# Kernel tuning notes

Measured on AMD Instinct MI355X. Metric: run time of the kernel, lower is better.

The kernel has to match this reference:

```python
import jax, jax.numpy as jnp
import numpy as np

EPS = 1e-12
SIMILARITY = 'dot'  # non-tensor forward arg, closed over


def setup_inputs() -> dict:
    key = jax.random.key(0)
    k1, k2, k3, k4 = jax.random.split(key, 4)
    N, M, D = 4096, 8192, 512
    x = jax.random.normal(k1, (N, D), dtype=jnp.float32)
    x_n = jax.random.normal(k2, (M, D), dtype=jnp.float32)
    # Linear(D, 3) params
    W = jax.random.normal(k3, (3, D), dtype=jnp.float32) * (1.0 / np.sqrt(D))
    bias = jax.random.normal(k4, (3,), dtype=jnp.float32) * 0.01
    return {"x": x, "x_n": x_n, "W": W, "bias": bias}


def _sim_matrix(x, x_n, similarity):
    if similarity == 'l2':
        d2 = (jnp.sum(x * x, 1)[:, None] - 2.0 * (x @ x_n.T)
              + jnp.sum(x_n * x_n, 1)[None, :])
        return -jnp.sqrt(jnp.maximum(d2, 0.0))
    elif similarity == 'l1':
        return -jnp.sum(jnp.abs(x[:, None, :] - x_n[None, :, :]), axis=-1)
    elif similarity == 'dot':
        return (x @ x_n.T) / x.shape[1]
    elif similarity == 'cos':
        xn = x / jnp.linalg.norm(x, axis=1, keepdims=True)
        yn = x_n / jnp.linalg.norm(x_n, axis=1, keepdims=True)
        return xn @ yn.T


def reference(x, x_n, W, bias):
    # pointwise params from a Linear(D,3)+Sigmoid head, clamped to (eps, 1-eps)
    p = jnp.clip(jax.nn.sigmoid(x @ W.T + bias), EPS, 1.0 - EPS)  # [N,3]
    a = p[:, 0:1]
    b = p[:, 1:2]
    s = p[:, 2:3]
    b = a + b * (1.0 - a)

    sim = _sim_matrix(x, x_n, SIMILARITY)                # [N,M]
    smin = jnp.min(sim, axis=1, keepdims=True)
    smax = jnp.max(sim, axis=1, keepdims=True)
    sim_norm = (sim - smin) / (smax - smin)

    # x != x_n -> plain row max (torch.equal branch is False)
    top_sims = jnp.max(sim_norm, axis=1, keepdims=True)  # [N,1]
    a = jnp.minimum(a, top_sims) - EPS

    num = jnp.maximum(jnp.abs(sim_norm - a) ** (1.0 / s), EPS)
    denom = num + jnp.maximum(jnp.abs(b - sim_norm) ** (1.0 / s), EPS)
    soft_mask = num / denom

    lo = sim_norm < a
    hi = sim_norm > b
    soft_mask = jnp.where(lo, 0.0, jnp.where(hi, 1.0, soft_mask))
    # safe log: masked-to-0 entries give -inf forward, zero grad (matches torch)
    safe = jnp.where(lo, 1.0, soft_mask)
    log_mask = jnp.where(lo, -jnp.inf, jnp.log(safe))
    return sim + log_mask
```

## Files before the change

### kernel.cpp

```cpp
#include <hip/hip_runtime.h>
#include <hip/hip_fp16.h>
#include <math.h>

#define EPSF 1e-12f
#define NEG_HUGE (-1e30f)

typedef _Float16 half8_t __attribute__((ext_vector_type(8)));
typedef _Float16 half4_t __attribute__((ext_vector_type(4)));
typedef float floatx4 __attribute__((ext_vector_type(4)));

__device__ __forceinline__ float sigmoid_stable(float v) {
    if (v >= 0.0f) {
        return 1.0f / (1.0f + expf(-v));
    } else {
        float e = expf(v);
        return e / (1.0f + e);
    }
}

__global__ __launch_bounds__(64) void row_params_kernel(
    const float* __restrict__ x, const float* __restrict__ W,
    const float* __restrict__ bias,
    float* __restrict__ aeff, float* __restrict__ bnew, float* __restrict__ tinv)
{
    const int r = blockIdx.x;
    const int l = threadIdx.x;
    const float* xr = x + (size_t)r * 512;
    float s0 = 0.0f, s1 = 0.0f, s2 = 0.0f;
#pragma unroll
    for (int i = 0; i < 8; ++i) {
        int e = l * 8 + i;
        float xv = xr[e];
        s0 = fmaf(xv, W[e], s0);
        s1 = fmaf(xv, W[512 + e], s1);
        s2 = fmaf(xv, W[1024 + e], s2);
    }
#pragma unroll
    for (int off = 32; off > 0; off >>= 1) {
        s0 += __shfl_xor(s0, off);
        s1 += __shfl_xor(s1, off);
        s2 += __shfl_xor(s2, off);
    }
    if (l == 0) {
        float p0 = fminf(fmaxf(sigmoid_stable(s0 + bias[0]), EPSF), 1.0f);
        float p1 = fminf(fmaxf(sigmoid_stable(s1 + bias[1]), EPSF), 1.0f);
        float p2 = fminf(fmaxf(sigmoid_stable(s2 + bias[2]), EPSF), 1.0f);
        float b = p0 + p1 * (1.0f - p0);
        float ae = fminf(p0, 1.0f) - EPSF;
        aeff[r] = ae;
        bnew[r] = b;
        tinv[r] = 1.0f / p2;
    }
}

__global__ __launch_bounds__(256) void split_both_kernel(
    const float* __restrict__ x, const float* __restrict__ xn,
    _Float16* __restrict__ A2, _Float16* __restrict__ B2)
{
    int idx = blockIdx.x * 256 + threadIdx.x;
    int row = idx >> 7;
    int c = (idx & 127) << 2;
    const float* src;
    _Float16* dst;
    bool isB;
    if (row < 4096) {
        src = x + (size_t)row * 512 + c;
        dst = A2 + (size_t)row * 1536 + c;
        isB = false;
    } else {
        int r = row - 4096;
        src = xn + (size_t)r * 512 + c;
        dst = B2 + (size_t)r * 1536 + c;
        isB = true;
    }
    float4 v = *(const float4*)src;
    _Float16 h0 = (_Float16)v.x, h1 = (_Float16)v.y,
             h2 = (_Float16)v.z, h3 = (_Float16)v.w;
    half4_t hv = {h0, h1, h2, h3};
    half4_t lv = {(_Float16)(v.x - (float)h0), (_Float16)(v.y - (float)h1),
                  (_Float16)(v.z - (float)h2), (_Float16)(v.w - (float)h3)};
    *(half4_t*)(dst) = hv;
    *(half4_t*)(dst + 512)  = isB ? lv : hv;
    *(half4_t*)(dst + 1024) = isB ? hv : lv;
}

__device__ __forceinline__ void load_tile_row16(
    const _Float16* gbase, _Float16* lds_base, int lane)
{
    const _Float16* g = gbase + (size_t)(lane >> 2) * 1536 + (size_t)(lane & 3) * 8;
    __builtin_amdgcn_global_load_lds(
        (const __attribute__((address_space(1))) unsigned int*)g,
        (__attribute__((address_space(3))) unsigned int*)lds_base,
        16, 0, 0);
}

__global__ __launch_bounds__(256) void mfma_gemm_kernel(
    const _Float16* __restrict__ A, const _Float16* __restrict__ B,
    float* __restrict__ C,
    float* __restrict__ pmin, float* __restrict__ pmax)
{
    constexpr int Kp = 1536;
    constexpr int N = 8192;
    __shared__ __align__(16) _Float16 As[128 * 32];
    __shared__ __align__(16) _Float16 Bs[128 * 32];

    const int t = threadIdx.x;
    const int wave = t >> 6;
    const int lane = t & 63;
    const int bx = blockIdx.x;
    const int by = blockIdx.y;

    const _Float16* Abase = A + (size_t)(by * 128 + wave * 16) * Kp;
    const _Float16* Bbase = B + (size_t)(bx * 128 + wave * 16) * Kp;
    _Float16* AsW0 = &As[(wave * 16) * 32];
    _Float16* AsW1 = &As[(64 + wave * 16) * 32];
    _Float16* BsW0 = &Bs[(wave * 16) * 32];
    _Float16* BsW1 = &Bs[(64 + wave * 16) * 32];
    const size_t rs64 = (size_t)64 * Kp;

    const int wm = (wave >> 1) * 64;
    const int wn = (wave & 1) * 64;
    const _Float16* aptr = &As[(wm + (lane & 15)) * 32 + (lane >> 4) * 8];
    const _Float16* bptr = &Bs[(wn + (lane & 15)) * 32 + (lane >> 4) * 8];

    floatx4 acc[4][4] = {};

    for (int kt = 0; kt < Kp / 32; ++kt) {
        const _Float16* Ak = Abase + kt * 32;
        const _Float16* Bk = Bbase + kt * 32;
        load_tile_row16(Ak, AsW0, lane);
        load_tile_row16(Ak + rs64, AsW1, lane);
        load_tile_row16(Bk, BsW0, lane);
        load_tile_row16(Bk + rs64, BsW1, lane);
        __syncthreads();

        half8_t af[4], bf[4];
#pragma unroll
        for (int i = 0; i < 4; ++i) af[i] = *(const half8_t*)(aptr + i * 16 * 32);
#pragma unroll
        for (int j = 0; j < 4; ++j) bf[j] = *(const half8_t*)(bptr + j * 16 * 32);
#pragma unroll
        for (int i = 0; i < 4; ++i)
#pragma unroll
            for (int j = 0; j < 4; ++j)
                acc[i][j] = __builtin_amdgcn_mfma_f32_16x16x32_f16(
                    af[i], bf[j], acc[i][j], 0, 0, 0);
        __syncthreads();
    }

    const float sc = 1.0f / 512.0f;
    const int row0 = by * 128 + wm + (lane >> 4) * 4;
    const int col0 = bx * 128 + wn + (lane & 15);
#pragma unroll
    for (int i = 0; i < 4; ++i) {
#pragma unroll
        for (int r = 0; r < 4; ++r) {
            float* cp = C + (size_t)(row0 + i * 16 + r) * N + col0;
#pragma unroll
            for (int j = 0; j < 4; ++j)
                cp[j * 16] = acc[i][j][r] * sc;
        }
    }

    float mnv[4][4], mxv[4][4];
#pragma unroll
    for (int i = 0; i < 4; ++i)
#pragma unroll
        for (int r = 0; r < 4; ++r) {
            float lo = fminf(fminf(acc[i][0][r], acc[i][1][r]),
                             fminf(acc[i][2][r], acc[i][3][r]));
            float hi = fmaxf(fmaxf(acc[i][0][r], acc[i][1][r]),
                             fmaxf(acc[i][2][r], acc[i][3][r]));
            mnv[i][r] = lo * sc;
            mxv[i][r] = hi * sc;
        }
#pragma unroll
    for (int off = 1; off < 16; off <<= 1)
#pragma unroll
        for (int i = 0; i < 4; ++i)
#pragma unroll
            for (int r = 0; r < 4; ++r) {
                mnv[i][r] = fminf(mnv[i][r], __shfl_xor(mnv[i][r], off));
                mxv[i][r] = fmaxf(mxv[i][r], __shfl_xor(mxv[i][r], off));
            }
    if ((lane & 15) == 0) {
        const int pb = bx * 2 + (wave & 1);
#pragma unroll
        for (int i = 0; i < 4; ++i)
#pragma unroll
            for (int r = 0; r < 4; ++r) {
                size_t row = (size_t)(row0 + i * 16 + r);
                pmin[(row << 7) + pb] = mnv[i][r];
                pmax[(row << 7) + pb] = mxv[i][r];
            }
    }
}

__global__ __launch_bounds__(64) void minmax_reduce_kernel(
    const float* __restrict__ pmin, const float* __restrict__ pmax,
    float* __restrict__ smin, float* __restrict__ smax)
{
    const int r = blockIdx.x;
    const int l = threadIdx.x;
    const float* bmin = pmin + ((size_t)r << 7);
    const float* bmax = pmax + ((size_t)r << 7);
    float mn = fminf(bmin[l], bmin[l + 64]);
    float mx = fmaxf(bmax[l], bmax[l + 64]);
#pragma unroll
    for (int off = 32; off > 0; off >>= 1) {
        mn = fminf(mn, __shfl_xor(mn, off));
        mx = fmaxf(mx, __shfl_xor(mx, off));
    }
    if (l == 0) {
        smin[r] = mn;
        smax[r] = mx;
    }
}

#define BM 128
#define BN 128
#define BK 16
__global__ __launch_bounds__(256) void sgemm_nt_kernel(
    const float* __restrict__ A, const float* __restrict__ B,
    float* __restrict__ C)
{
    const int K = 512;
    const int N = 8192;
    __shared__ float As[BK][BM];
    __shared__ float Bs[BK][BN];
    const int t = threadIdx.x;
    const int bx = blockIdx.x, by = blockIdx.y;
    const int m0 = t >> 2;
    const int kq = (t & 3) << 2;
    const float* Ap = A + ((size_t)(by * BM + m0) * K + kq);
    const float* Bp = B + ((size_t)(bx * BN + m0) * K + kq);
    const int tx = t & 15, ty = t >> 4;
    float acc[8][8] = {};
    float4 a0 = *(const float4*)(Ap), a1 = *(const float4*)(Ap + (size_t)64 * K);
    float4 b0 = *(const float4*)(Bp), b1 = *(const float4*)(Bp + (size_t)64 * K);
    for (int kt = 0; kt < K / BK; ++kt) {
        As[kq + 0][m0] = a0.x; As[kq + 1][m0] = a0.y; As[kq + 2][m0] = a0.z; As[kq + 3][m0] = a0.w;
        As[kq + 0][m0 + 64] = a1.x; As[kq + 1][m0 + 64] = a1.y; As[kq + 2][m0 + 64] = a1.z; As[kq + 3][m0 + 64] = a1.w;
        Bs[kq + 0][m0] = b0.x; Bs[kq + 1][m0] = b0.y; Bs[kq + 2][m0] = b0.z; Bs[kq + 3][m0] = b0.w;
        Bs[kq + 0][m0 + 64] = b1.x; Bs[kq + 1][m0 + 64] = b1.y; Bs[kq + 2][m0 + 64] = b1.z; Bs[kq + 3][m0 + 64] = b1.w;
        __syncthreads();
        if (kt + 1 < K / BK) {
            const float* Ap2 = Ap + (size_t)(kt + 1) * BK;
            const float* Bp2 = Bp + (size_t)(kt + 1) * BK;
            a0 = *(const float4*)(Ap2); a1 = *(const float4*)(Ap2 + (size_t)64 * K);
            b0 = *(const float4*)(Bp2); b1 = *(const float4*)(Bp2 + (size_t)64 * K);
        }
#pragma unroll
        for (int k = 0; k < BK; ++k) {
            float4 xa0 = *(const float4*)(&As[k][ty * 8]);
            float4 xa1 = *(const float4*)(&As[k][ty * 8 + 4]);
            float4 yb0 = *(const float4*)(&Bs[k][tx * 8]);
            float4 yb1 = *(const float4*)(&Bs[k][tx * 8 + 4]);
            float av[8] = {xa0.x, xa0.y, xa0.z, xa0.w, xa1.x, xa1.y, xa1.z, xa1.w};
            float bv[8] = {yb0.x, yb0.y, yb0.z, yb0.w, yb1.x, yb1.y, yb1.z, yb1.w};
#pragma unroll
            for (int i = 0; i < 8; ++i)
#pragma unroll
                for (int j = 0; j < 8; ++j)
                    acc[i][j] = fmaf(av[i], bv[j], acc[i][j]);
        }
        __syncthreads();
    }
    const float sc = 1.0f / 512.0f;
    const int gm = by * BM + ty * 8, gn = bx * BN + tx * 8;
#pragma unroll
    for (int i = 0; i < 8; ++i) {
        float4 o0 = make_float4(acc[i][0] * sc, acc[i][1] * sc, acc[i][2] * sc, acc[i][3] * sc);
        float4 o1 = make_float4(acc[i][4] * sc, acc[i][5] * sc, acc[i][6] * sc, acc[i][7] * sc);
        float* cp = C + (size_t)(gm + i) * N + gn;
        *(float4*)(cp) = o0;
        *(float4*)(cp + 4) = o1;
    }
}

__global__ __launch_bounds__(256) void row_minmax_kernel(
    const float* __restrict__ C, float* __restrict__ smin, float* __restrict__ smax)
{
    const int r = blockIdx.x;
    const float4* row = (const float4*)(C + (size_t)r * 8192);
    float mn = INFINITY, mx = -INFINITY;
#pragma unroll
    for (int i = 0; i < 8; ++i) {
        float4 v = row[threadIdx.x + i * 256];
        mn = fminf(mn, fminf(fminf(v.x, v.y), fminf(v.z, v.w)));
        mx = fmaxf(mx, fmaxf(fmaxf(v.x, v.y), fmaxf(v.z, v.w)));
    }
#pragma unroll
    for (int off = 32; off > 0; off >>= 1) {
        mn = fminf(mn, __shfl_xor(mn, off));
        mx = fmaxf(mx, __shfl_xor(mx, off));
    }
    __shared__ float smn[4], smx[4];
    if ((threadIdx.x & 63) == 0) {
        smn[threadIdx.x >> 6] = mn;
        smx[threadIdx.x >> 6] = mx;
    }
    __syncthreads();
    if (threadIdx.x == 0) {
        mn = fminf(fminf(smn[0], smn[1]), fminf(smn[2], smn[3]));
        mx = fmaxf(fmaxf(smx[0], smx[1]), fmaxf(smx[2], smx[3]));
        smin[r] = mn;
        smax[r] = mx;
    }
}

__device__ __forceinline__ float fast_pow(float x, float t) {
    return __expf(t * __logf(x));
}

__global__ __launch_bounds__(256) void epilogue_kernel(
    float* __restrict__ C,
    const float* __restrict__ aeff, const float* __restrict__ bnew,
    const float* __restrict__ tinv,
    const float* __restrict__ smin, const float* __restrict__ smax)
{
    const int r = blockIdx.y;
    const int c4 = blockIdx.x * 256 + threadIdx.x;
    const float a = aeff[r];
    const float b = bnew[r];
    const float t = tinv[r];
    const float mn = smin[r];
    const float range = smax[r] - mn;
    const float inv_range = (range > 0.0f) ? (1.0f / range) : 0.0f;

    floatx4* p = (floatx4*)(C + (size_t)r * 8192) + c4;
    floatx4 v = __builtin_nontemporal_load(p);
    floatx4 out;
#pragma unroll
    for (int i = 0; i < 4; ++i) {
        float sim = v[i];
        float sn = (sim - mn) * inv_range;
        float lm;
        if (sn < a) {
            lm = NEG_HUGE;
        } else if (sn > b) {
            lm = 0.0f;
        } else {
            float num = fmaxf(fast_pow(fabsf(sn - a), t), EPSF);
            float den = num + fmaxf(fast_pow(fabsf(b - sn), t), EPSF);
            lm = __logf(num / den);
        }
        out[i] = sim + lm;
    }
    __builtin_nontemporal_store(out, p);
}

extern "C" void kernel_launch(void* const* d_in, const int* in_sizes, int n_in,
                              void* d_out, int out_size, void* d_ws, size_t ws_size,
                              hipStream_t stream)
{
    const float* x    = (const float*)d_in[0];
    const float* x_n  = (const float*)d_in[1];
    const float* W    = (const float*)d_in[2];
    const float* bias = (const float*)d_in[3];
    float* C = (float*)d_out;
    float* ws = (float*)d_ws;

    float* aeff = ws;
    float* bnew = ws + 4096;
    float* tinv = ws + 8192;
    float* smin = ws + 12288;
    float* smax = ws + 16384;

    const size_t pmin_off = 128 * 1024;
    const size_t pbytes = (size_t)4096 * 128 * 4;
    const size_t a2_off = pmin_off + 2 * pbytes;
    const size_t a2_bytes = (size_t)4096 * 1536 * 2;
    const size_t b2_off = a2_off + a2_bytes;
    const size_t need = b2_off + (size_t)8192 * 1536 * 2;

    row_params_kernel<<<4096, 64, 0, stream>>>(x, W, bias, aeff, bnew, tinv);

    if (ws_size >= need) {
        float* pmin = (float*)((char*)d_ws + pmin_off);
        float* pmax = (float*)((char*)d_ws + pmin_off + pbytes);
        _Float16* A2 = (_Float16*)((char*)d_ws + a2_off);
        _Float16* B2 = (_Float16*)((char*)d_ws + b2_off);
        split_both_kernel<<<6144, 256, 0, stream>>>(x, x_n, A2, B2);
        mfma_gemm_kernel<<<dim3(64, 32), 256, 0, stream>>>(A2, B2, C, pmin, pmax);
        minmax_reduce_kernel<<<4096, 64, 0, stream>>>(pmin, pmax, smin, smax);
    } else {
        sgemm_nt_kernel<<<dim3(8192 / BN, 4096 / BM), 256, 0, stream>>>(x, x_n, C);
        row_minmax_kernel<<<4096, 256, 0, stream>>>(C, smin, smax);
    }

    epilogue_kernel<<<dim3(8, 4096), 256, 0, stream>>>(C, aeff, bnew, tinv,
                                                       smin, smax);
}
```

Before: 327.9 us.

## Rewrite split-fp16 MFMA GEMM as 256x256 double-buffered pipelined kernel

```diff
diff --git a/kernel.cpp b/kernel.cpp
--- a/kernel.cpp
+++ b/kernel.cpp
@@ -84,115 +84,146 @@
     *(half4_t*)(dst + 1024) = isB ? hv : lv;
 }
 
-__device__ __forceinline__ void load_tile_row16(
-    const _Float16* gbase, _Float16* lds_base, int lane)
-{
-    const _Float16* g = gbase + (size_t)(lane >> 2) * 1536 + (size_t)(lane & 3) * 8;
+#define VMW_(N) asm volatile("s_waitcnt vmcnt(" #N ")" ::: "memory")
+#define VMW(N) VMW_(N)
+#define BARR() asm volatile("s_barrier" ::: "memory")
+#define LGKM0() asm volatile("s_waitcnt lgkmcnt(0)" ::: "memory")
+
+__device__ __forceinline__ void gload16(const _Float16* g, _Float16* l) {
     __builtin_amdgcn_global_load_lds(
         (const __attribute__((address_space(1))) unsigned int*)g,
-        (__attribute__((address_space(3))) unsigned int*)lds_base,
-        16, 0, 0);
-}
-
-__global__ __launch_bounds__(256) void mfma_gemm_kernel(
+        (__attribute__((address_space(3))) unsigned int*)l, 16, 0, 0);
+}
+
+#define PHASE(FMB, STAGES, VMN, DOREADB, Q)                                    \
+    {                                                                          \
+        if (DOREADB) {                                                         \
+            const _Float16* bb = lds + (Q) * 16384 + BrdW;                     \
+            _Pragma("unroll")                                                  \
+            for (int fn = 0; fn < 4; ++fn) {                                   \
+                bfr[fn][0] = *(const half8_t*)(bb + fn * 1024 + g0);           \
+                bfr[fn][1] = *(const half8_t*)(bb + fn * 1024 + g1);           \
+            }                                                                  \
+        }                                                                      \
+        const _Float16* ab = lds + (Q) * 16384 + ArdW;                         \
+        half8_t af0k0 = *(const half8_t*)(ab + (FMB) * 1024 + g0);             \
+        half8_t af0k1 = *(const half8_t*)(ab + (FMB) * 1024 + g1);             \
+        half8_t af1k0 = *(const half8_t*)(ab + ((FMB) + 1) * 1024 + g0);       \
+        half8_t af1k1 = *(const half8_t*)(ab + ((FMB) + 1) * 1024 + g1);       \
+        STAGES;                                                                \
+        BARR();                                                                \
+        LGKM0();                                                               \
+        __builtin_amdgcn_s_setprio(1);                                         \
+        _Pragma("unroll")                                                      \
+        for (int fn = 0; fn < 4; ++fn) {                                       \
+            acc[FMB][fn] = __builtin_amdgcn_mfma_f32_16x16x32_f16(             \
+                af0k0, bfr[fn][0], acc[FMB][fn], 0, 0, 0);                     \
+            acc[FMB][fn] = __builtin_amdgcn_mfma_f32_16x16x32_f16(             \
+                af0k1, bfr[fn][1], acc[FMB][fn], 0, 0, 0);                     \
+            acc[(FMB) + 1][fn] = __builtin_amdgcn_mfma_f32_16x16x32_f16(       \
+                af1k0, bfr[fn][0], acc[(FMB) + 1][fn], 0, 0, 0);               \
+            acc[(FMB) + 1][fn] = __builtin_amdgcn_mfma_f32_16x16x32_f16(       \
+                af1k1, bfr[fn][1], acc[(FMB) + 1][fn], 0, 0, 0);               \
+        }                                                                      \
+        __builtin_amdgcn_s_setprio(0);                                         \
+        VMW(VMN);                                                              \
+        BARR();                                                                \
+    }
+
+__global__ __launch_bounds__(512) void mfma_gemm256_kernel(
     const _Float16* __restrict__ A, const _Float16* __restrict__ B,
     float* __restrict__ C,
     float* __restrict__ pmin, float* __restrict__ pmax)
 {
-    constexpr int Kp = 1536;
-    constexpr int N = 8192;
-    __shared__ __align__(16) _Float16 As[128 * 32];
-    __shared__ __align__(16) _Float16 Bs[128 * 32];
-
-    const int t = threadIdx.x;
-    const int wave = t >> 6;
-    const int lane = t & 63;
+    constexpr int KP = 1536;
+    constexpr int NN = 8192;
+    constexpr int NT = KP / 64;
+    __shared__ __align__(16) _Float16 lds[65536];
+
+    const int tid = threadIdx.x;
+    const int wave = tid >> 6, lane = tid & 63;
     const int bx = blockIdx.x;
     const int by = blockIdx.y;
-
-    const _Float16* Abase = A + (size_t)(by * 128 + wave * 16) * Kp;
-    const _Float16* Bbase = B + (size_t)(bx * 128 + wave * 16) * Kp;
-    _Float16* AsW0 = &As[(wave * 16) * 32];
-    _Float16* AsW1 = &As[(64 + wave * 16) * 32];
-    _Float16* BsW0 = &Bs[(wave * 16) * 32];
-    _Float16* BsW1 = &Bs[(64 + wave * 16) * 32];
-    const size_t rs64 = (size_t)64 * Kp;
-
-    const int wm = (wave >> 1) * 64;
-    const int wn = (wave & 1) * 64;
-    const _Float16* aptr = &As[(wm + (lane & 15)) * 32 + (lane >> 4) * 8];
-    const _Float16* bptr = &Bs[(wn + (lane & 15)) * 32 + (lane >> 4) * 8];
-
-    floatx4 acc[4][4] = {};
-
-    for (int kt = 0; kt < Kp / 32; ++kt) {
-        const _Float16* Ak = Abase + kt * 32;
-        const _Float16* Bk = Bbase + kt * 32;
-        load_tile_row16(Ak, AsW0, lane);
-        load_tile_row16(Ak + rs64, AsW1, lane);
-        load_tile_row16(Bk, BsW0, lane);
-        load_tile_row16(Bk + rs64, BsW1, lane);
-        __syncthreads();
-
-        half8_t af[4], bf[4];
-#pragma unroll
-        for (int i = 0; i < 4; ++i) af[i] = *(const half8_t*)(aptr + i * 16 * 32);
-#pragma unroll
-        for (int j = 0; j < 4; ++j) bf[j] = *(const half8_t*)(bptr + j * 16 * 32);
-#pragma unroll
-        for (int i = 0; i < 4; ++i)
-#pragma unroll
-            for (int j = 0; j < 4; ++j)
-                acc[i][j] = __builtin_amdgcn_mfma_f32_16x16x32_f16(
-                    af[i], bf[j], acc[i][j], 0, 0, 0);
-        __syncthreads();
-    }
+    const int wm = (wave >> 2) * 128;
+    const int wn = (wave & 3) * 64;
+
+    const int rl = lane & 15, lq = lane >> 4;
+    const int rx7 = lane & 7;
+    const int lrow = lane >> 3, gph = lane & 7;
+    const int glog = gph ^ lrow;
+
+    const _Float16* Bg = B + (size_t)(bx * 256 + wave * 8 + lrow) * KP + glog * 8;
+    const _Float16* Ag = A + (size_t)(by * 256 + ((wave & 4) ? 128 : 0)
+                                      + (wave & 3) * 8 + lrow) * KP + glog * 8;
+    const int BdstW = 32768 + (wave * 8) * 64;
+    const int AdstW = (((wave & 4) ? 128 : 0) + (wave & 3) * 8) * 64;
+    const int ArdW = (wm + rl) * 64;
+    const int BrdW = 32768 + (wn + rl) * 64;
+    const int g0 = (lq ^ rx7) * 8;
+    const int g1 = ((4 + lq) ^ rx7) * 8;
+
+    floatx4 acc[8][4] = {};
+    half8_t bfr[4][2];
+
+    auto stageB = [&](int u, int qn, int kn) {
+        gload16(Bg + (size_t)u * (64 * KP) + kn * 64,
+                lds + qn * 16384 + BdstW + u * 4096);
+    };
+    auto stageA = [&](int s, int qn, int kn) {
+        gload16(Ag + (size_t)s * (32 * KP) + kn * 64,
+                lds + qn * 16384 + AdstW + s * 2048);
+    };
+
+#pragma unroll
+    for (int u = 0; u < 4; ++u) stageB(u, 0, 0);
+#pragma unroll
+    for (int s = 0; s < 4; ++s) stageA(s, 0, 0);
+    VMW(3);
+    BARR();
+
+    for (int kt = 0; kt < NT - 1; ++kt) {
+        const int q = kt & 1, qn = q ^ 1, kn = kt + 1;
+        PHASE(0, (stageB(0, qn, kn), stageB(1, qn, kn)), 4, true, q);
+        PHASE(2, (stageB(2, qn, kn), stageB(3, qn, kn)), 5, false, q);
+        PHASE(4, (stageA(0, qn, kn), stageA(1, qn, kn)), 6, false, q);
+        PHASE(6, (stageA(2, qn, kn), stageA(3, qn, kn)), 3, false, q);
+    }
+    PHASE(0, (void)0, 2, true, 1);
+    PHASE(2, (void)0, 1, false, 1);
+    PHASE(4, (void)0, 0, false, 1);
+    PHASE(6, (void)0, 63, false, 1);
 
     const float sc = 1.0f / 512.0f;
-    const int row0 = by * 128 + wm + (lane >> 4) * 4;
-    const int col0 = bx * 128 + wn + (lane & 15);
-#pragma unroll
-    for (int i = 0; i < 4; ++i) {
+    const int row0 = by * 256 + wm + lq * 4;
+    const int col0 = bx * 256 + wn + rl;
+    const int pslot = bx * 4 + (wave & 3);
+#pragma unroll
+    for (int fm = 0; fm < 8; ++fm) {
+        float mn[4], mx[4];
 #pragma unroll
         for (int r = 0; r < 4; ++r) {
-            float* cp = C + (size_t)(row0 + i * 16 + r) * N + col0;
-#pragma unroll
-            for (int j = 0; j < 4; ++j)
-                cp[j * 16] = acc[i][j][r] * sc;
+            float* cp = C + (size_t)(row0 + fm * 16 + r) * NN + col0;
+            float v0 = acc[fm][0][r] * sc, v1 = acc[fm][1][r] * sc;
+            float v2 = acc[fm][2][r] * sc, v3 = acc[fm][3][r] * sc;
+            cp[0] = v0; cp[16] = v1; cp[32] = v2; cp[48] = v3;
+            mn[r] = fminf(fminf(v0, v1), fminf(v2, v3));
+            mx[r] = fmaxf(fmaxf(v0, v1), fmaxf(v2, v3));
         }
-    }
-
-    float mnv[4][4], mxv[4][4];
-#pragma unroll
-    for (int i = 0; i < 4; ++i)
-#pragma unroll
-        for (int r = 0; r < 4; ++r) {
-            float lo = fminf(fminf(acc[i][0][r], acc[i][1][r]),
-                             fminf(acc[i][2][r], acc[i][3][r]));
-            float hi = fmaxf(fmaxf(acc[i][0][r], acc[i][1][r]),
-                             fmaxf(acc[i][2][r], acc[i][3][r]));
-            mnv[i][r] = lo * sc;
-            mxv[i][r] = hi * sc;
+#pragma unroll
+        for (int off = 1; off < 16; off <<= 1)
+#pragma unroll
+            for (int r = 0; r < 4; ++r) {
+                mn[r] = fminf(mn[r], __shfl_xor(mn[r], off));
+                mx[r] = fmaxf(mx[r], __shfl_xor(mx[r], off));
+            }
+        if (rl == 0) {
+#pragma unroll
+            for (int r = 0; r < 4; ++r) {
+                size_t row = (size_t)(row0 + fm * 16 + r);
+                pmin[(row << 7) + pslot] = mn[r];
+                pmax[(row << 7) + pslot] = mx[r];
+            }
         }
-#pragma unroll
-    for (int off = 1; off < 16; off <<= 1)
-#pragma unroll
-        for (int i = 0; i < 4; ++i)
-#pragma unroll
-            for (int r = 0; r < 4; ++r) {
-                mnv[i][r] = fminf(mnv[i][r], __shfl_xor(mnv[i][r], off));
-                mxv[i][r] = fmaxf(mxv[i][r], __shfl_xor(mxv[i][r], off));
-            }
-    if ((lane & 15) == 0) {
-        const int pb = bx * 2 + (wave & 1);
-#pragma unroll
-        for (int i = 0; i < 4; ++i)
-#pragma unroll
-            for (int r = 0; r < 4; ++r) {
-                size_t row = (size_t)(row0 + i * 16 + r);
-                pmin[(row << 7) + pb] = mnv[i][r];
-                pmax[(row << 7) + pb] = mxv[i][r];
-            }
     }
 }
 
@@ -382,7 +413,7 @@
         _Float16* A2 = (_Float16*)((char*)d_ws + a2_off);
         _Float16* B2 = (_Float16*)((char*)d_ws + b2_off);
         split_both_kernel<<<6144, 256, 0, stream>>>(x, x_n, A2, B2);
-        mfma_gemm_kernel<<<dim3(64, 32), 256, 0, stream>>>(A2, B2, C, pmin, pmax);
+        mfma_gemm256_kernel<<<dim3(32, 16), 512, 0, stream>>>(A2, B2, C, pmin, pmax);
         minmax_reduce_kernel<<<4096, 64, 0, stream>>>(pmin, pmax, smin, smax);
     } else {
         sgemm_nt_kernel<<<dim3(8192 / BN, 4096 / BM), 256, 0, stream>>>(x, x_n, C);
```

Result: faster. 297.1 us (-9.4%).
